# Performance work log

Hardware: AMD Instinct MI355X
Metric: run time of the kernel (lower is better)

Reference implementation:

```python
import jax, jax.numpy as jnp
import numpy as np

N_HEADS = 16

def setup_inputs() -> dict:
    key = jax.random.key(0)
    qkv = jax.random.normal(key, (8, 3072, 1024), dtype=jnp.float32)
    return {"qkv": qkv}

def reference(qkv) -> jnp.ndarray:
    B, D, L = qkv.shape
    q, k, v = jnp.split(qkv, 3, axis=1)            # each [B, H*ch, L]
    ch = D // (3 * N_HEADS)
    scale = 1.0 / np.sqrt(np.sqrt(ch)).astype(np.float32)
    q = (q * scale).reshape(B * N_HEADS, ch, L)
    k = (k * scale).reshape(B * N_HEADS, ch, L)
    v = v.reshape(B * N_HEADS, ch, L)
    weight = jnp.einsum('bct,bcs->bts', q, k)       # [B*H, L, L]
    weight = jax.nn.softmax(weight, axis=-1)
    z = jnp.einsum('bts,bcs->bct', weight, v)       # [B*H, ch, L]
    return z.reshape(B, -1, L)
```

## Files before the change

kernel.cpp:

```cpp
#include <hip/hip_runtime.h>


typedef __attribute__((ext_vector_type(8))) _Float16 f16x8;
typedef __attribute__((ext_vector_type(4))) _Float16 f16x4;
typedef __attribute__((ext_vector_type(4))) float f32x4;

#define MAT_HALVES 8388608
#define WS_BYTES   33554432

#define ASYNC16(g, l) __builtin_amdgcn_global_load_lds(                    \
    (__attribute__((address_space(1))) void*)(void*)(g),                   \
    (__attribute__((address_space(3))) void*)(void*)(l), 16, 0, 0)

__global__ __launch_bounds__(256) void prepass_kv(
    const float* __restrict__ qkv, _Float16* __restrict__ ws) {
    __shared__ float ft[64][68];
    const int tid = threadIdx.x;
    const int bid = blockIdx.x;
    const int mat = bid >> 11;
    const int idx = bid & 2047;
    const int head = idx >> 4;
    const int blk  = idx & 15;
    const int b = head >> 4, h = head & 15;
    const float* src = qkv + (size_t)b * 3072 * 1024
                           + (size_t)((1 + mat) * 1024 + h * 64) * 1024;
    const int s0 = blk * 64;
    if (mat == 0) {
#pragma unroll
        for (int i = 0; i < 4; ++i) {
            const int c = i * 16 + (tid >> 4);
            const int s = (tid & 15) * 4;
            const float4 v = *(const float4*)(src + (size_t)c * 1024 + s0 + s);
            ft[s + 0][c] = v.x;
            ft[s + 1][c] = v.y;
            ft[s + 2][c] = v.z;
            ft[s + 3][c] = v.w;
        }
        __syncthreads();
        _Float16* dst = ws + (size_t)head * 65536 + (size_t)s0 * 64;
#pragma unroll
        for (int r = 0; r < 2; ++r) {
            const int g = r * 256 + tid;
            const int t = g >> 3, cb = g & 7;
            const float4 a = *(const float4*)&ft[t][cb * 8];
            const float4 bq = *(const float4*)&ft[t][cb * 8 + 4];
            f16x8 o = { (_Float16)a.x,  (_Float16)a.y,  (_Float16)a.z,  (_Float16)a.w,
                        (_Float16)bq.x, (_Float16)bq.y, (_Float16)bq.z, (_Float16)bq.w };
            *(f16x8*)(dst + (size_t)t * 64 + (size_t)(cb ^ (t & 7)) * 8) = o;
        }
    } else {
        _Float16* dst = ws + (size_t)MAT_HALVES + (size_t)head * 65536;
#pragma unroll
        for (int i = 0; i < 4; ++i) {
            const int c = i * 16 + (tid >> 4);
            const int s = (tid & 15) * 4;
            const float4 v = *(const float4*)(src + (size_t)c * 1024 + s0 + s);
            f16x4 o = { (_Float16)v.x, (_Float16)v.y, (_Float16)v.z, (_Float16)v.w };
            const int sb = s >> 3, pos = s & 7;
            *(f16x4*)(dst + (size_t)c * 1024 + s0 + (size_t)((sb ^ (c & 7)) * 8 + pos)) = o;
        }
    }
}

__launch_bounds__(512, 4)
__global__ void attn_kernel(const float* __restrict__ qkv,
                            const _Float16* __restrict__ ws,
                            float* __restrict__ out) {
    __shared__ __align__(16) union SM {
        _Float16 kv[2][8192];
        float ft[64][68];
    } sm;

    const int tid  = threadIdx.x;
    const int wv   = tid >> 6;
    const int lane = tid & 63;
    const int li   = lane & 15;
    const int quad = lane >> 4;

    const int bid  = blockIdx.x;
    const int head = (bid >> 5) * 8 + (bid & 7);
    const int tt   = (bid >> 3) & 3;
    const int t0   = tt * 256;

    const int b = head >> 4, h = head & 15;
    const float* qsrc = qkv + (size_t)b * 3072 * 1024 + (size_t)(h * 64) * 1024;
    const _Float16* kt = ws + (size_t)head * 65536;
    const _Float16* vh = ws + (size_t)MAT_HALVES + (size_t)head * 65536;

    const float qscale = 0.125f * 1.44269504f;
    f16x8 bqf[2][2];
    {
        const int ci = tid >> 4;
        const int tq = (tid & 15) * 4;
        for (int ct = 0; ct < 4; ++ct) {
#pragma unroll
            for (int i = 0; i < 2; ++i) {
                const int c = i * 32 + ci;
                const float4 v = *(const float4*)(qsrc + (size_t)c * 1024 + t0 + ct * 64 + tq);
                sm.ft[tq + 0][c] = v.x * qscale;
                sm.ft[tq + 1][c] = v.y * qscale;
                sm.ft[tq + 2][c] = v.z * qscale;
                sm.ft[tq + 3][c] = v.w * qscale;
            }
            __syncthreads();
            if ((wv >> 1) == ct) {
#pragma unroll
                for (int sub = 0; sub < 2; ++sub) {
                    const int tl = (wv & 1) * 32 + sub * 16 + li;
#pragma unroll
                    for (int kk = 0; kk < 2; ++kk) {
                        const int c0 = (kk * 4 + quad) * 8;
                        const float4 a  = *(const float4*)&sm.ft[tl][c0];
                        const float4 b2 = *(const float4*)&sm.ft[tl][c0 + 4];
                        bqf[sub][kk] = f16x8{ (_Float16)a.x,  (_Float16)a.y,
                                              (_Float16)a.z,  (_Float16)a.w,
                                              (_Float16)b2.x, (_Float16)b2.y,
                                              (_Float16)b2.z, (_Float16)b2.w };
                    }
                }
            }
            __syncthreads();
        }
    }

    ASYNC16(kt + (size_t)tid * 8, &sm.kv[0][tid * 8]);
    ASYNC16(vh + (size_t)(tid >> 3) * 1024 + (size_t)(tid & 7) * 8,
            &sm.kv[0][4096 + tid * 8]);

    f32x4 accz[2][4] = {};
    float psum[2] = {};

    for (int si = 0; si < 16; ++si) {
        __syncthreads();
        if (si < 15) {
            const int s0n = (si + 1) * 64;
            const int nb = (si + 1) & 1;
            ASYNC16(kt + (size_t)s0n * 64 + (size_t)tid * 8, &sm.kv[nb][tid * 8]);
            ASYNC16(vh + (size_t)(tid >> 3) * 1024 + s0n + (size_t)(tid & 7) * 8,
                    &sm.kv[nb][4096 + tid * 8]);
        }
        const _Float16* Kl = &sm.kv[si & 1][0];
        const _Float16* Vl = &sm.kv[si & 1][4096];

#pragma unroll
        for (int ns = 0; ns < 4; ++ns) {
            f16x8 ak[2];
#pragma unroll
            for (int kk = 0; kk < 2; ++kk) {
                const int cb = (kk * 4 + quad) ^ (li & 7);
                ak[kk] = *(const f16x8*)&Kl[(ns * 16 + li) * 64 + cb * 8];
            }
            f16x4 pk[2];
#pragma unroll
            for (int sub = 0; sub < 2; ++sub) {
                f32x4 st = {};
                st = __builtin_amdgcn_mfma_f32_16x16x32_f16(ak[0], bqf[sub][0], st, 0, 0, 0);
                st = __builtin_amdgcn_mfma_f32_16x16x32_f16(ak[1], bqf[sub][1], st, 0, 0, 0);
                const float p0 = __builtin_amdgcn_exp2f(st[0]);
                const float p1 = __builtin_amdgcn_exp2f(st[1]);
                const float p2 = __builtin_amdgcn_exp2f(st[2]);
                const float p3 = __builtin_amdgcn_exp2f(st[3]);
                psum[sub] += (p0 + p1) + (p2 + p3);
                pk[sub] = f16x4{ (_Float16)p0, (_Float16)p1,
                                 (_Float16)p2, (_Float16)p3 };
            }
            const int sb  = 2 * ns + (quad >> 1);
            const int pos = (quad & 1) * 4;
#pragma unroll
            for (int nc = 0; nc < 4; ++nc) {
                const int c = nc * 16 + li;
                f16x4 bv = *(const f16x4*)&Vl[c * 64 + ((sb ^ (c & 7)) << 3) + pos];
                accz[0][nc] = __builtin_amdgcn_mfma_f32_16x16x16f16(
                    pk[0], bv, accz[0][nc], 0, 0, 0);
                accz[1][nc] = __builtin_amdgcn_mfma_f32_16x16x16f16(
                    pk[1], bv, accz[1][nc], 0, 0, 0);
            }
        }
    }

    float rl[2][4];
#pragma unroll
    for (int sub = 0; sub < 2; ++sub) {
        float s = psum[sub];
        s += __shfl_xor(s, 16);
        s += __shfl_xor(s, 32);
#pragma unroll
        for (int r = 0; r < 4; ++r)
            rl[sub][r] = 1.0f / __shfl(s, quad * 4 + r);
    }

    float* obase = out + (size_t)b * 1024 * 1024
                       + (size_t)(h * 64) * 1024 + t0;
#pragma unroll
    for (int sub = 0; sub < 2; ++sub)
#pragma unroll
        for (int nc = 0; nc < 4; ++nc) {
            const int c = nc * 16 + li;
            const int t = wv * 32 + sub * 16 + quad * 4;
            f32x4 z = accz[sub][nc];
            float4 o = { z[0] * rl[sub][0], z[1] * rl[sub][1],
                         z[2] * rl[sub][2], z[3] * rl[sub][3] };
            *(float4*)(obase + (size_t)c * 1024 + t) = o;
        }
}

struct S1fb {
    _Float16 K[64][72];
    _Float16 V[64][72];
    _Float16 P[128][72];
};
union SMemFb {
    S1fb s1;
    float zt[64][132];
};

__launch_bounds__(256, 4)
__global__ void qkv_attn_fallback(const float* __restrict__ qkv,
                                  float* __restrict__ out) {
    constexpr int L = 1024;
    __shared__ SMemFb sm;
    const int tid  = threadIdx.x;
    const int wv   = tid >> 6;
    const int lane = tid & 63;
    const int li   = lane & 15;
    const int quad = lane >> 4;
    const int bid  = blockIdx.x;
    const int head = (bid >> 6) * 8 + (bid & 7);
    const int tt   = (bid >> 3) & 7;
    const int b = head >> 4;
    const int h = head & 15;
    const float* qbase = qkv + (size_t)b * 3072 * L + (size_t)(h * 64) * L;
    const float* kbase = qbase + (size_t)1024 * L;
    const float* vbase = qbase + (size_t)2048 * L;
    float*       obase = out + (size_t)b * 1024 * L + (size_t)(h * 64) * L;
    const int t0 = tt * 128;
#pragma unroll
    for (int i = 0; i < 4; ++i) {
        const int c = i * 16 + (tid >> 4);
        const int t = (tid & 15) * 8;
        const float4 qa = *(const float4*)(qbase + (size_t)c * L + t0 + t);
        const float4 qb = *(const float4*)(qbase + (size_t)c * L + t0 + t + 4);
        sm.s1.P[t + 0][c] = (_Float16)(qa.x * 0.125f);
        sm.s1.P[t + 1][c] = (_Float16)(qa.y * 0.125f);
        sm.s1.P[t + 2][c] = (_Float16)(qa.z * 0.125f);
        sm.s1.P[t + 3][c] = (_Float16)(qa.w * 0.125f);
        sm.s1.P[t + 4][c] = (_Float16)(qb.x * 0.125f);
        sm.s1.P[t + 5][c] = (_Float16)(qb.y * 0.125f);
        sm.s1.P[t + 6][c] = (_Float16)(qb.z * 0.125f);
        sm.s1.P[t + 7][c] = (_Float16)(qb.w * 0.125f);
    }
    __syncthreads();
    f16x8 aq0[2], aq1[2];
#pragma unroll
    for (int kk = 0; kk < 2; ++kk) {
        aq0[kk] = *(const f16x8*)&sm.s1.P[wv * 32 + li][kk * 32 + quad * 8];
        aq1[kk] = *(const f16x8*)&sm.s1.P[wv * 32 + 16 + li][kk * 32 + quad * 8];
    }
    f32x4 accz0[4] = {}, accz1[4] = {};
    float psum0[4] = {}, psum1[4] = {};
    float4 kreg[4], vreg[4];
#pragma unroll
    for (int i = 0; i < 4; ++i) {
        const int c = i * 16 + (tid >> 4);
        const int s = (tid & 15) * 4;
        kreg[i] = *(const float4*)(kbase + (size_t)c * L + s);
        vreg[i] = *(const float4*)(vbase + (size_t)c * L + s);
    }
    for (int si = 0; si < 16; ++si) {
        __syncthreads();
#pragma unroll
        for (int i = 0; i < 4; ++i) {
            const int c = i * 16 + (tid >> 4);
            const int s = (tid & 15) * 4;
            sm.s1.K[s + 0][c] = (_Float16)kreg[i].x;
            sm.s1.K[s + 1][c] = (_Float16)kreg[i].y;
            sm.s1.K[s + 2][c] = (_Float16)kreg[i].z;
            sm.s1.K[s + 3][c] = (_Float16)kreg[i].w;
            f16x4 pv = { (_Float16)vreg[i].x, (_Float16)vreg[i].y,
                         (_Float16)vreg[i].z, (_Float16)vreg[i].w };
            *(f16x4*)&sm.s1.V[c][s] = pv;
        }
        __syncthreads();
        if (si < 15) {
            const int s0n = (si + 1) * 64;
#pragma unroll
            for (int i = 0; i < 4; ++i) {
                const int c = i * 16 + (tid >> 4);
                const int s = (tid & 15) * 4;
                kreg[i] = *(const float4*)(kbase + (size_t)c * L + s0n + s);
                vreg[i] = *(const float4*)(vbase + (size_t)c * L + s0n + s);
            }
        }
#pragma unroll
        for (int nt = 0; nt < 4; ++nt) {
            f32x4 a0 = {}, a1 = {};
#pragma unroll
            for (int kk = 0; kk < 2; ++kk) {
                f16x8 bk = *(const f16x8*)&sm.s1.K[nt * 16 + li][kk * 32 + quad * 8];
                a0 = __builtin_amdgcn_mfma_f32_16x16x32_f16(aq0[kk], bk, a0, 0, 0, 0);
                a1 = __builtin_amdgcn_mfma_f32_16x16x32_f16(aq1[kk], bk, a1, 0, 0, 0);
            }
#pragma unroll
            for (int r = 0; r < 4; ++r) {
                const float p0 = __expf(a0[r]);
                const float p1 = __expf(a1[r]);
                psum0[r] += p0;
                psum1[r] += p1;
                sm.s1.P[wv * 32 + quad * 4 + r][nt * 16 + li] = (_Float16)p0;
                sm.s1.P[wv * 32 + 16 + quad * 4 + r][nt * 16 + li] = (_Float16)p1;
            }
        }
#pragma unroll
        for (int kk = 0; kk < 2; ++kk) {
            f16x8 ap0 = *(const f16x8*)&sm.s1.P[wv * 32 + li][kk * 32 + quad * 8];
            f16x8 ap1 = *(const f16x8*)&sm.s1.P[wv * 32 + 16 + li][kk * 32 + quad * 8];
#pragma unroll
            for (int nt = 0; nt < 4; ++nt) {
                f16x8 bv = *(const f16x8*)&sm.s1.V[nt * 16 + li][kk * 32 + quad * 8];
                accz0[nt] = __builtin_amdgcn_mfma_f32_16x16x32_f16(ap0, bv, accz0[nt], 0, 0, 0);
                accz1[nt] = __builtin_amdgcn_mfma_f32_16x16x32_f16(ap1, bv, accz1[nt], 0, 0, 0);
            }
        }
    }
    float rl0[4], rl1[4];
#pragma unroll
    for (int r = 0; r < 4; ++r) {
        float s0 = psum0[r], s1 = psum1[r];
        s0 += __shfl_xor(s0, 1); s0 += __shfl_xor(s0, 2);
        s0 += __shfl_xor(s0, 4); s0 += __shfl_xor(s0, 8);
        s1 += __shfl_xor(s1, 1); s1 += __shfl_xor(s1, 2);
        s1 += __shfl_xor(s1, 4); s1 += __shfl_xor(s1, 8);
        rl0[r] = 1.0f / s0;
        rl1[r] = 1.0f / s1;
    }
    __syncthreads();
#pragma unroll
    for (int nt = 0; nt < 4; ++nt)
#pragma unroll
        for (int r = 0; r < 4; ++r) {
            sm.zt[nt * 16 + li][wv * 32 + quad * 4 + r]      = accz0[nt][r] * rl0[r];
            sm.zt[nt * 16 + li][wv * 32 + 16 + quad * 4 + r] = accz1[nt][r] * rl1[r];
        }
    __syncthreads();
#pragma unroll
    for (int i = 0; i < 8; ++i) {
        const int c = i * 8 + (tid >> 5);
        const int t = (tid & 31) * 4;
        float4 o = { sm.zt[c][t], sm.zt[c][t + 1],
                     sm.zt[c][t + 2], sm.zt[c][t + 3] };
        *(float4*)(obase + (size_t)c * L + t0 + t) = o;
    }
}

extern "C" void kernel_launch(void* const* d_in, const int* in_sizes, int n_in,
                              void* d_out, int out_size, void* d_ws, size_t ws_size,
                              hipStream_t stream) {
    const float* qkv = (const float*)d_in[0];
    float* out = (float*)d_out;
    if (ws_size >= (size_t)WS_BYTES) {
        _Float16* ws = (_Float16*)d_ws;
        prepass_kv<<<4096, 256, 0, stream>>>(qkv, ws);
        attn_kernel<<<512, 512, 0, stream>>>(qkv, ws, out);
    } else {
        qkv_attn_fallback<<<1024, 256, 0, stream>>>(qkv, out);
    }
}
```

Baseline: 195.9 us.

## Split key dimension across two wave groups with LDS reduction in attention kernel

The attention block grows from 512 to 1024 threads. Two groups of 8 waves each handle half of the 64-key sub-tiles per step, and the partial PV accumulators and row sums are combined through shared memory in a two-phase epilogue. The first K/V tile is now prefetched before the Q transpose so the two overlap, and s_setprio is raised around the MFMA section. This adds wave-level parallelism per tile and splits K and V loading between the groups, at the cost of a reduction epilogue, extra barriers and more LDS per block.

```diff
diff --git a/kernel.cpp b/kernel.cpp
--- a/kernel.cpp
+++ b/kernel.cpp
@@ -62,17 +62,19 @@
     }
 }
 
-__launch_bounds__(512, 4)
+__launch_bounds__(1024, 8)
 __global__ void attn_kernel(const float* __restrict__ qkv,
                             const _Float16* __restrict__ ws,
                             float* __restrict__ out) {
     __shared__ __align__(16) union SM {
-        _Float16 kv[2][8192];
-        float ft[64][68];
+        struct { _Float16 kv[2][8192]; float ft[64][68]; } m;
+        struct { float z[4][64][33]; float ps[4][64][2]; } ep;
     } sm;
 
     const int tid  = threadIdx.x;
     const int wv   = tid >> 6;
+    const int tg   = wv & 7;
+    const int sg   = wv >> 3;
     const int lane = tid & 63;
     const int li   = lane & 15;
     const int quad = lane >> 4;
@@ -87,31 +89,38 @@
     const _Float16* kt = ws + (size_t)head * 65536;
     const _Float16* vh = ws + (size_t)MAT_HALVES + (size_t)head * 65536;
 
+    const int g = tg * 64 + lane;
+#pragma unroll
+    for (int u = 0; u < 2; ++u) {
+        if (sg == 0) {
+            ASYNC16(kt + (size_t)u * 4096 + (size_t)g * 8, &sm.m.kv[u][g * 8]);
+        } else {
+            ASYNC16(vh + (size_t)(g >> 3) * 1024 + u * 64 + (size_t)(g & 7) * 8,
+                    &sm.m.kv[u][4096 + g * 8]);
+        }
+    }
+
     const float qscale = 0.125f * 1.44269504f;
     f16x8 bqf[2][2];
     {
-        const int ci = tid >> 4;
-        const int tq = (tid & 15) * 4;
+        const int ci  = tid >> 4;
+        const int tq4 = (tid & 15) * 4;
         for (int ct = 0; ct < 4; ++ct) {
-#pragma unroll
-            for (int i = 0; i < 2; ++i) {
-                const int c = i * 32 + ci;
-                const float4 v = *(const float4*)(qsrc + (size_t)c * 1024 + t0 + ct * 64 + tq);
-                sm.ft[tq + 0][c] = v.x * qscale;
-                sm.ft[tq + 1][c] = v.y * qscale;
-                sm.ft[tq + 2][c] = v.z * qscale;
-                sm.ft[tq + 3][c] = v.w * qscale;
-            }
+            const float4 v = *(const float4*)(qsrc + (size_t)ci * 1024 + t0 + ct * 64 + tq4);
+            sm.m.ft[tq4 + 0][ci] = v.x * qscale;
+            sm.m.ft[tq4 + 1][ci] = v.y * qscale;
+            sm.m.ft[tq4 + 2][ci] = v.z * qscale;
+            sm.m.ft[tq4 + 3][ci] = v.w * qscale;
             __syncthreads();
-            if ((wv >> 1) == ct) {
+            if ((tg >> 1) == ct) {
 #pragma unroll
                 for (int sub = 0; sub < 2; ++sub) {
-                    const int tl = (wv & 1) * 32 + sub * 16 + li;
+                    const int tl = (tg & 1) * 32 + sub * 16 + li;
 #pragma unroll
                     for (int kk = 0; kk < 2; ++kk) {
                         const int c0 = (kk * 4 + quad) * 8;
-                        const float4 a  = *(const float4*)&sm.ft[tl][c0];
-                        const float4 b2 = *(const float4*)&sm.ft[tl][c0 + 4];
+                        const float4 a  = *(const float4*)&sm.m.ft[tl][c0];
+                        const float4 b2 = *(const float4*)&sm.m.ft[tl][c0 + 4];
                         bqf[sub][kk] = f16x8{ (_Float16)a.x,  (_Float16)a.y,
                                               (_Float16)a.z,  (_Float16)a.w,
                                               (_Float16)b2.x, (_Float16)b2.y,
@@ -123,10 +132,6 @@
         }
     }
 
-    ASYNC16(kt + (size_t)tid * 8, &sm.kv[0][tid * 8]);
-    ASYNC16(vh + (size_t)(tid >> 3) * 1024 + (size_t)(tid & 7) * 8,
-            &sm.kv[0][4096 + tid * 8]);
-
     f32x4 accz[2][4] = {};
     float psum[2] = {};
 
@@ -134,16 +139,21 @@
         __syncthreads();
         if (si < 15) {
             const int s0n = (si + 1) * 64;
-            const int nb = (si + 1) & 1;
-            ASYNC16(kt + (size_t)s0n * 64 + (size_t)tid * 8, &sm.kv[nb][tid * 8]);
-            ASYNC16(vh + (size_t)(tid >> 3) * 1024 + s0n + (size_t)(tid & 7) * 8,
-                    &sm.kv[nb][4096 + tid * 8]);
-        }
-        const _Float16* Kl = &sm.kv[si & 1][0];
-        const _Float16* Vl = &sm.kv[si & 1][4096];
-
-#pragma unroll
-        for (int ns = 0; ns < 4; ++ns) {
+            const int nb  = (si + 1) & 1;
+            if (sg == 0) {
+                ASYNC16(kt + (size_t)s0n * 64 + (size_t)g * 8, &sm.m.kv[nb][g * 8]);
+            } else {
+                ASYNC16(vh + (size_t)(g >> 3) * 1024 + s0n + (size_t)(g & 7) * 8,
+                        &sm.m.kv[nb][4096 + g * 8]);
+            }
+        }
+        const _Float16* Kl = &sm.m.kv[si & 1][0];
+        const _Float16* Vl = &sm.m.kv[si & 1][4096];
+
+        __builtin_amdgcn_s_setprio(1);
+#pragma unroll
+        for (int n2 = 0; n2 < 2; ++n2) {
+            const int ns = sg * 2 + n2;
             f16x8 ak[2];
 #pragma unroll
             for (int kk = 0; kk < 2; ++kk) {
@@ -176,32 +186,60 @@
                     pk[1], bv, accz[1][nc], 0, 0, 0);
             }
         }
-    }
-
-    float rl[2][4];
-#pragma unroll
-    for (int sub = 0; sub < 2; ++sub) {
-        float s = psum[sub];
-        s += __shfl_xor(s, 16);
-        s += __shfl_xor(s, 32);
-#pragma unroll
-        for (int r = 0; r < 4; ++r)
-            rl[sub][r] = 1.0f / __shfl(s, quad * 4 + r);
+        __builtin_amdgcn_s_setprio(0);
     }
 
     float* obase = out + (size_t)b * 1024 * 1024
                        + (size_t)(h * 64) * 1024 + t0;
-#pragma unroll
-    for (int sub = 0; sub < 2; ++sub)
-#pragma unroll
-        for (int nc = 0; nc < 4; ++nc) {
-            const int c = nc * 16 + li;
-            const int t = wv * 32 + sub * 16 + quad * 4;
-            f32x4 z = accz[sub][nc];
-            float4 o = { z[0] * rl[sub][0], z[1] * rl[sub][1],
-                         z[2] * rl[sub][2], z[3] * rl[sub][3] };
-            *(float4*)(obase + (size_t)c * 1024 + t) = o;
-        }
+    __syncthreads();
+#pragma unroll
+    for (int ph = 0; ph < 2; ++ph) {
+        if (sg == 1 && (tg >> 2) == ph) {
+            const int tz = tg & 3;
+#pragma unroll
+            for (int sub = 0; sub < 2; ++sub)
+#pragma unroll
+                for (int nc = 0; nc < 4; ++nc)
+                    *(f32x4*)&sm.ep.z[tz][lane][sub * 16 + nc * 4] = accz[sub][nc];
+            sm.ep.ps[tz][lane][0] = psum[0];
+            sm.ep.ps[tz][lane][1] = psum[1];
+        }
+        __syncthreads();
+        if (sg == 0 && (tg >> 2) == ph) {
+            const int tz = tg & 3;
+            psum[0] += sm.ep.ps[tz][lane][0];
+            psum[1] += sm.ep.ps[tz][lane][1];
+#pragma unroll
+            for (int sub = 0; sub < 2; ++sub)
+#pragma unroll
+                for (int nc = 0; nc < 4; ++nc) {
+                    const f32x4 zp = *(const f32x4*)&sm.ep.z[tz][lane][sub * 16 + nc * 4];
+                    accz[sub][nc] += zp;
+                }
+            float rl[2][4];
+#pragma unroll
+            for (int sub = 0; sub < 2; ++sub) {
+                float s = psum[sub];
+                s += __shfl_xor(s, 16);
+                s += __shfl_xor(s, 32);
+#pragma unroll
+                for (int r = 0; r < 4; ++r)
+                    rl[sub][r] = 1.0f / __shfl(s, quad * 4 + r);
+            }
+#pragma unroll
+            for (int sub = 0; sub < 2; ++sub)
+#pragma unroll
+                for (int nc = 0; nc < 4; ++nc) {
+                    const int c = nc * 16 + li;
+                    const int t = tg * 32 + sub * 16 + quad * 4;
+                    f32x4 z = accz[sub][nc];
+                    float4 o = { z[0] * rl[sub][0], z[1] * rl[sub][1],
+                                 z[2] * rl[sub][2], z[3] * rl[sub][3] };
+                    *(float4*)(obase + (size_t)c * 1024 + t) = o;
+                }
+        }
+        __syncthreads();
+    }
 }
 
 struct S1fb {
@@ -360,7 +398,7 @@
     if (ws_size >= (size_t)WS_BYTES) {
         _Float16* ws = (_Float16*)d_ws;
         prepass_kv<<<4096, 256, 0, stream>>>(qkv, ws);
-        attn_kernel<<<512, 512, 0, stream>>>(qkv, ws, out);
+        attn_kernel<<<512, 1024, 0, stream>>>(qkv, ws, out);
     } else {
         qkv_attn_fallback<<<1024, 256, 0, stream>>>(qkv, out);
     }
```

New measurement: 403.9 us. +106.2%, slower.
